# Performance work log

Hardware: AMD Instinct MI355X
Metric: run time of the kernel (lower is better)

## Reference

```python
import jax, jax.numpy as jnp
import numpy as np

B, S, D = 8, 4096, 192
MEM_READ, MEM_WRITE, MEM_READY = 156, 157, 158


def setup_inputs() -> dict:
    key = jax.random.key(0)
    ks = jax.random.split(key, 9)
    inp = {"x": jax.random.normal(ks[0], (B, S, D), dtype=jnp.float32)}
    names = ["Wq_r", "Wk_r", "Wv_r", "Wo_r", "Wq_w", "Wk_w", "Wv_w", "Wo_w"]
    for i, n in enumerate(names):
        inp[n] = jax.random.normal(ks[i + 1], (D, D), dtype=jnp.float32) * 0.02
    return inp


def _attention(x, Wq, Wk, Wv, Wo):
    # single-head, non-causal PureAttention: q/k/v = x @ W.T, softmax(qk^T/sqrt(D)) v, then W_o
    q = jnp.einsum('bsd,ed->bse', x, Wq)
    k = jnp.einsum('bsd,ed->bse', x, Wk)
    v = jnp.einsum('bsd,ed->bse', x, Wv)
    scale = jnp.asarray(1.0 / np.sqrt(D), x.dtype)
    scores = jnp.einsum('bqe,bke->bqk', q, k) * scale  # [B,S,S]
    attn = jax.nn.softmax(scores, axis=-1)
    o = jnp.einsum('bqk,bke->bqe', attn, v)
    return jnp.einsum('bse,oe->bso', o, Wo)


def reference(x, Wq_r, Wk_r, Wv_r, Wo_r, Wq_w, Wk_w, Wv_w, Wo_w):
    read_flag = x[:, 0, MEM_READ]    # [B]
    write_flag = x[:, 0, MEM_WRITE]  # [B]
    read_res = _attention(x, Wq_r, Wk_r, Wv_r, Wo_r)
    write_res = _attention(x, Wq_w, Wk_w, Wv_w, Wo_w)
    rg = read_flag[:, None, None]
    wg = write_flag[:, None, None]
    out = x + rg * (read_res - x) + wg * (write_res - x)
    out = out.at[:, :, MEM_READ].set(0.0)
    out = out.at[:, :, MEM_WRITE].set(0.0)
    ready = (read_flag + write_flag)[:, None]  # broadcast over seq
    out = out.at[:, :, MEM_READY].set(jnp.broadcast_to(ready, out.shape[:2]))
    return out
```

## Files before the change

kernel.cpp:

```cpp
#include <hip/hip_runtime.h>
#include <stdint.h>

#define B_ 8
#define S_ 4096
#define D_ 192
#define M_ (B_*S_)

typedef short v8s __attribute__((ext_vector_type(8)));
typedef float v4f __attribute__((ext_vector_type(4)));
typedef unsigned short v4us __attribute__((ext_vector_type(4)));
typedef unsigned long long ull;

static __device__ __forceinline__ unsigned short f2bf(float f){
  union{float f; unsigned u;} v; v.f=f;
  unsigned u = v.u;
  unsigned r = (u + 0x7fffu + ((u>>16)&1u))>>16;
  return (unsigned short)r;
}
static __device__ __forceinline__ float fexp2(float x){
  return __builtin_amdgcn_exp2f(x);
}
static __device__ __forceinline__ unsigned cvtpk(float lo, float hi){
  unsigned r;
  asm("v_cvt_pk_bf16_f32 %0, %1, %2" : "=v"(r) : "v"(lo), "v"(hi));
  return r;
}

static __device__ __forceinline__ unsigned sw_fp8(float x){
  union{float f; unsigned u;} v; v.f = x;
  unsigned s = (v.u >> 24) & 0x80u;
  float a = fabsf(x);
  if (a < 0.001953125f) return s;
  if (a >= 240.f) return s | 0x7Eu;
  if (a < 0.015625f) {
    int m = (int)(a*512.f + 0.5f); if(m>7) m=7;
    return s | (unsigned)m;
  }
  int e = (int)((v.u >> 23) & 0xff) - 127;
  unsigned mant = (v.u >> 20) & 0x7u;
  unsigned rest = v.u & 0xFFFFFu;
  if (rest > 0x80000u || (rest == 0x80000u && (mant&1u))) mant++;
  unsigned ee = (unsigned)(e + 7);
  if (mant == 8u){ mant = 0u; ee++; }
  return s | (ee<<3) | mant;
}
template<bool HI>
static __device__ __forceinline__ unsigned pk8(float a, float b, unsigned old){
#if __has_builtin(__builtin_amdgcn_cvt_pk_fp8_f32)
  return __builtin_amdgcn_cvt_pk_fp8_f32(a, b, old, HI);
#else
  unsigned p = sw_fp8(a) | (sw_fp8(b)<<8);
  return HI ? ((old & 0x0000FFFFu) | (p<<16)) : ((old & 0xFFFF0000u) | p);
#endif
}

typedef const __attribute__((address_space(1))) unsigned int gu32;
typedef __attribute__((address_space(3))) unsigned int lu32;
#define GLL16(gp, lp) __builtin_amdgcn_global_load_lds((gu32*)(gp), (lu32*)(lp), 16, 0, 0)

__global__ void cvt_w_kernel(const float* w0,const float* w1,const float* w2,const float* w3,
                             const float* w4,const float* w5,const float* w6,const float* w7,
                             unsigned short* dst){
  int w = blockIdx.y;
  const float* src;
  switch(w){
    case 0: src=w0; break; case 1: src=w1; break; case 2: src=w2; break; case 3: src=w3; break;
    case 4: src=w4; break; case 5: src=w5; break; case 6: src=w6; break; default: src=w7; break;
  }
  int i = blockIdx.x*256 + threadIdx.x;
  float v = src[i];
  if(w==0 || w==4 || w==1 || w==5) v *= 0.32267249f;
  dst[(size_t)w*36864 + i] = f2bf(v);
}

__global__ __launch_bounds__(256) void proj_kernel(
    const float* __restrict__ x, const unsigned short* __restrict__ Wb,
    unsigned char* __restrict__ QK8, unsigned short* __restrict__ V16)
{
  __shared__ __align__(16) unsigned short Vstage[192*72];
  const size_t MDB = (size_t)M_*D_;
  const size_t MD  = (size_t)M_*D_;
  int tid = threadIdx.x;
  int wid = tid>>6, lane = tid&63;
  int lr = lane&15, lg = lane>>4, kb = lg*8;
  int m0 = blockIdx.x*64 + wid*16;
  int row = m0 + lr;

  v8s a[6];
  #pragma unroll
  for(int c=0;c<6;c++){
    const float* xp = &x[(size_t)row*D_ + c*32 + kb];
    float4 f0 = *(const float4*)xp;
    float4 f1 = *(const float4*)(xp+4);
    v8s t;
    t[0]=(short)f2bf(f0.x); t[1]=(short)f2bf(f0.y); t[2]=(short)f2bf(f0.z); t[3]=(short)f2bf(f0.w);
    t[4]=(short)f2bf(f1.x); t[5]=(short)f2bf(f1.y); t[6]=(short)f2bf(f1.z); t[7]=(short)f2bf(f1.w);
    a[c]=t;
  }
  int bidx = m0 / S_;
  int sb   = (blockIdx.x*64) % S_;
  int sloc = wid*16 + lg*4;

  for(int path=0; path<2; path++){
    unsigned char* dstQ8 = QK8 + (size_t)path*2*MDB;
    for(int which=0; which<2; which++){
      const unsigned short* W = Wb + (size_t)(path*4 + which)*36864;
      unsigned char* dst = which==0 ? dstQ8 : dstQ8 + MDB;
      #pragma unroll
      for(int nt=0; nt<12; nt++){
        v4f acc = {0.f,0.f,0.f,0.f};
        int n = nt*16 + lr;
        #pragma unroll
        for(int c=0;c<6;c++){
          v8s bfr = *(const v8s*)&W[(size_t)n*D_ + c*32 + kb];
          acc = __builtin_amdgcn_mfma_f32_16x16x32_bf16(a[c], bfr, acc, 0,0,0);
        }
        int col = nt*16 + lr;
        int r0 = m0 + lg*4;
        #pragma unroll
        for(int r=0;r<4;r++){
          unsigned p = pk8<false>(acc[r], 0.f, 0u);
          dst[(size_t)(r0+r)*D_ + col] = (unsigned char)(p & 0xFF);
        }
      }
    }
    {
      const unsigned short* W = Wb + (size_t)(path*4 + 2)*36864;
      #pragma unroll
      for(int nt=0; nt<12; nt++){
        v4f acc = {0.f,0.f,0.f,0.f};
        int n = nt*16 + lr;
        #pragma unroll
        for(int c=0;c<6;c++){
          v8s bfr = *(const v8s*)&W[(size_t)n*D_ + c*32 + kb];
          acc = __builtin_amdgcn_mfma_f32_16x16x32_bf16(a[c], bfr, acc, 0,0,0);
        }
        int col = nt*16 + lr;
        v4us pk;
        pk[0]=f2bf(acc[0]); pk[1]=f2bf(acc[1]); pk[2]=f2bf(acc[2]); pk[3]=f2bf(acc[3]);
        *(v4us*)&Vstage[col*72 + sloc] = pk;
      }
      __syncthreads();
      unsigned short* dstV = V16 + (size_t)path*MD;
      size_t vg = (size_t)bidx*D_*S_ + sb;
      #pragma unroll
      for(int j=0;j<6;j++){
        int i = tid + j*256;
        int d = i>>3, s8 = (i&7)*8;
        *(v8s*)&dstV[vg + (size_t)d*S_ + s8] = *(const v8s*)&Vstage[d*72 + s8];
      }
      __syncthreads();
    }
  }
}

#define KSTR8 200

__global__ __launch_bounds__(256,3) void attn_kernel(
    const unsigned char* __restrict__ QK8,
    const unsigned short* __restrict__ V16,
    unsigned short* __restrict__ Ob)
{
  __shared__ __align__(16) unsigned char  KL[2][32*KSTR8];
  __shared__ __align__(16) unsigned short VL[2][192*32];

  int flat = blockIdx.x + 32*blockIdx.y + 256*blockIdx.z;
  int w = (flat&7)*64 + (flat>>3);
  int qi = w & 31;
  int b  = (w>>5) & 7;
  int z  = w>>8;

  const size_t MDB = (size_t)M_*D_;
  const unsigned char* Q8 = QK8 + (size_t)z*2*MDB;
  const unsigned char* K8 = Q8 + MDB;
  const unsigned short* Vt = V16 + (size_t)z*M_*D_;
  unsigned short* O = Ob + (size_t)z*M_*D_;

  int q0 = qi*128;
  int tid = threadIdx.x, wid=tid>>6, lane=tid&63;
  int lr = lane&15, lg = lane>>4;
  size_t bK = (size_t)b*S_*D_;
  size_t bV = (size_t)b*D_*S_;
  int qrow0 = q0 + wid*32;

  int ksR = tid>>3, ksC = (tid&7)*24;
  int kLds = ksR*KSTR8 + ksC;
  int voff[3], vLds[3];
  #pragma unroll
  for(int j=0;j<3;j++){
    int i = tid + j*256;
    int vrow = i>>2, vin = (i&3)*16;
    voff[j] = vrow*4096 + ((vin ^ (((vrow>>1)&3)<<4))>>1);
    vLds[j] = i*16;
  }
  int vro = ((lg*16) ^ (((lr>>1)&3)<<4)) >> 1;

  long qf8[2][6];
  #pragma unroll
  for(int h=0;h<2;h++){
    const unsigned char* qp = Q8 + bK + (size_t)(qrow0 + h*16 + lr)*D_;
    #pragma unroll
    for(int c=0;c<6;c++) qf8[h][c] = *(const long*)(qp + c*32 + lg*8);
  }
  float lsum[2] = {0.f, 0.f};
  v4f oacc[2][12];
  #pragma unroll
  for(int h=0;h<2;h++)
    #pragma unroll
    for(int e=0;e<12;e++) oacc[h][e] = (v4f){0.f,0.f,0.f,0.f};

  ull kreg0, kreg1, kreg2;
  auto kissue = [&](int t){
    const unsigned char* kg = K8 + bK + (size_t)t*6144 + ksR*192 + ksC;
    kreg0 = *(const ull*)(kg);
    kreg1 = *(const ull*)(kg+8);
    kreg2 = *(const ull*)(kg+16);
  };
  auto kwrite = [&](int buf){
    unsigned char* d = &KL[buf][kLds];
    *(ull*)(d)    = kreg0;
    *(ull*)(d+8)  = kreg1;
    *(ull*)(d+16) = kreg2;
  };
  auto vissue = [&](int t, int buf){
    const unsigned short* vg = Vt + bV + (size_t)t*32;
    #pragma unroll
    for(int j=0;j<3;j++) GLL16(vg + voff[j], ((unsigned char*)&VL[buf][0]) + vLds[j]);
  };
  auto do_qk = [&](int kcur, v4f sacc[2][2]){
    __builtin_amdgcn_s_setprio(1);
    #pragma unroll
    for(int ct=0; ct<2; ct++){
      v4f s0 = {0.f,0.f,0.f,0.f}, s1 = {0.f,0.f,0.f,0.f};
      const unsigned char* rb = &KL[kcur][(ct*16+lr)*KSTR8];
      #pragma unroll
      for(int c=0;c<6;c++){
        long kf8 = *(const long*)(rb + c*32 + lg*8);
        s0 = __builtin_amdgcn_mfma_f32_16x16x32_fp8_fp8(kf8, qf8[0][c], s0, 0,0,0);
        s1 = __builtin_amdgcn_mfma_f32_16x16x32_fp8_fp8(kf8, qf8[1][c], s1, 0,0,0);
      }
      sacc[0][ct]=s0; sacc[1][ct]=s1;
    }
    __builtin_amdgcn_s_setprio(0);
  };
  auto do_softmax = [&](v4f sacc[2][2], v8s pa[2]){
    #pragma unroll
    for(int h=0;h<2;h++){
      float p00=fexp2(sacc[h][0][0]), p01=fexp2(sacc[h][0][1]);
      float p02=fexp2(sacc[h][0][2]), p03=fexp2(sacc[h][0][3]);
      float p10=fexp2(sacc[h][1][0]), p11=fexp2(sacc[h][1][1]);
      float p12=fexp2(sacc[h][1][2]), p13=fexp2(sacc[h][1][3]);
      lsum[h] += ((p00+p01)+(p02+p03)) + ((p10+p11)+(p12+p13));
      unsigned X0=cvtpk(p00,p01), X1=cvtpk(p02,p03);
      unsigned Y0=cvtpk(p10,p11), Y1=cvtpk(p12,p13);
      asm("v_permlane32_swap_b32 %0, %1" : "+v"(Y0), "+v"(X0));
      asm("v_permlane32_swap_b32 %0, %1" : "+v"(Y1), "+v"(X1));
      asm("v_permlane16_swap_b32 %0, %1" : "+v"(Y0), "+v"(X0));
      asm("v_permlane16_swap_b32 %0, %1" : "+v"(Y1), "+v"(X1));
      union{ v8s s; unsigned w[4]; } u;
      u.w[0] = X0;  u.w[1] = X1;  u.w[2] = Y0;  u.w[3] = Y1;
      pa[h] = u.s;
    }
  };
  auto do_pv = [&](int vcur, v8s pa[2]){
    __builtin_amdgcn_s_setprio(1);
    #pragma unroll
    for(int e=0;e<12;e++){
      v8s vbf = *(const v8s*)&VL[vcur][(e*16+lr)*32 + vro];
      oacc[0][e] = __builtin_amdgcn_mfma_f32_16x16x32_bf16(pa[0], vbf, oacc[0][e], 0,0,0);
      oacc[1][e] = __builtin_amdgcn_mfma_f32_16x16x32_bf16(pa[1], vbf, oacc[1][e], 0,0,0);
    }
    __builtin_amdgcn_s_setprio(0);
  };

  kissue(0);
  vissue(0, 0);
  kwrite(0);
  asm volatile("s_waitcnt vmcnt(0)" ::: "memory");
  __syncthreads();

  for(int t=0; t<128; t++){
    int cur = t&1;
    if(t<127){ kissue(t+1); vissue(t+1, cur^1); }
    __builtin_amdgcn_sched_barrier(0);

    v4f sacc[2][2];
    do_qk(cur, sacc);
    v8s pa[2];
    do_softmax(sacc, pa);
    do_pv(cur, pa);

    if(t<127) kwrite(cur^1);
    asm volatile("s_waitcnt vmcnt(0)" ::: "memory");
    __syncthreads();
  }

  float invr[2][4];
  #pragma unroll
  for(int h=0;h<2;h++){
    float ps = lsum[h];
    ps += __shfl_xor(ps, 16);
    ps += __shfl_xor(ps, 32);
    float iv = 1.0f/ps;
    #pragma unroll
    for(int r=0;r<4;r++) invr[h][r] = __shfl(iv, lg*4+r, 16);
  }
  #pragma unroll
  for(int h=0;h<2;h++){
    size_t orow0 = ((size_t)b*S_ + qrow0 + h*16 + lg*4)*D_;
    #pragma unroll
    for(int e=0;e<12;e++){
      #pragma unroll
      for(int r=0;r<4;r++){
        O[orow0 + (size_t)r*D_ + e*16 + lr] = f2bf(oacc[h][e][r]*invr[h][r]);
      }
    }
  }
}

__global__ __launch_bounds__(256) void final_kernel(
  const float* __restrict__ x,
  const unsigned short* __restrict__ Or,
  const unsigned short* __restrict__ Ow,
  const unsigned short* __restrict__ WoR,
  const unsigned short* __restrict__ WoW,
  float* __restrict__ out)
{
  int tid=threadIdx.x, wid=tid>>6, lane=tid&63;
  int lr=lane&15, lg=lane>>4, kb=lg*8;
  int m0 = blockIdx.x*64 + wid*16;
  int arow = m0 + lr;
  v8s ar[6], aw[6];
  #pragma unroll
  for(int c=0;c<6;c++){
    ar[c] = *(const v8s*)&Or[(size_t)arow*D_ + c*32 + kb];
    aw[c] = *(const v8s*)&Ow[(size_t)arow*D_ + c*32 + kb];
  }
  int bidx = m0 / S_;
  float rf = x[(size_t)bidx*S_*D_ + 156];
  float wf = x[(size_t)bidx*S_*D_ + 157];
  #pragma unroll
  for(int nt=0; nt<12; nt++){
    v4f accR={0.f,0.f,0.f,0.f}, accW={0.f,0.f,0.f,0.f};
    int n = nt*16 + lr;
    #pragma unroll
    for(int c=0;c<6;c++){
      v8s br = *(const v8s*)&WoR[(size_t)n*D_ + c*32 + kb];
      accR = __builtin_amdgcn_mfma_f32_16x16x32_bf16(ar[c], br, accR,0,0,0);
      v8s bw = *(const v8s*)&WoW[(size_t)n*D_ + c*32 + kb];
      accW = __builtin_amdgcn_mfma_f32_16x16x32_bf16(aw[c], bw, accW,0,0,0);
    }
    #pragma unroll
    for(int r=0;r<4;r++){
      int row = m0 + lg*4 + r;
      int col = nt*16 + lr;
      float xv = x[(size_t)row*D_ + col];
      float val = xv + rf*(accR[r]-xv) + wf*(accW[r]-xv);
      if(col==156||col==157) val = 0.f;
      else if(col==158) val = rf+wf;
      out[(size_t)row*D_ + col] = val;
    }
  }
}

extern "C" void kernel_launch(void* const* d_in, const int* in_sizes, int n_in,
                              void* d_out, int out_size, void* d_ws, size_t ws_size,
                              hipStream_t stream) {
  const float* x = (const float*)d_in[0];
  char* wsb = (char*)d_ws;
  const size_t WSZ = 36864;
  const size_t MDB = (size_t)M_*D_;
  unsigned short* Wb  = (unsigned short*)wsb;
  unsigned char*  QK8 = (unsigned char*)(wsb + 8*WSZ*2);
  unsigned short* V16 = (unsigned short*)(wsb + 8*WSZ*2 + 4*MDB);
  unsigned short* Ob  = V16 + 2*MDB;

  cvt_w_kernel<<<dim3(144,8),256,0,stream>>>(
      (const float*)d_in[1],(const float*)d_in[2],(const float*)d_in[3],(const float*)d_in[4],
      (const float*)d_in[5],(const float*)d_in[6],(const float*)d_in[7],(const float*)d_in[8], Wb);

  proj_kernel<<<512,256,0,stream>>>(x, Wb, QK8, V16);
  attn_kernel<<<dim3(32,8,2),256,0,stream>>>(QK8, V16, Ob);
  final_kernel<<<512,256,0,stream>>>(x, Ob, Ob + MDB,
                                     Wb+3*WSZ, Wb+7*WSZ, (float*)d_out);
}
```

Baseline: 354.4 us.

## Split attention over two key halves and combine partials in final kernel

```diff
diff --git a/kernel.cpp b/kernel.cpp
--- a/kernel.cpp
+++ b/kernel.cpp
@@ -16,6 +16,9 @@
   unsigned u = v.u;
   unsigned r = (u + 0x7fffu + ((u>>16)&1u))>>16;
   return (unsigned short)r;
+}
+static __device__ __forceinline__ float bf2f(short s){
+  union{unsigned u; float f;} v; v.u = ((unsigned)(unsigned short)s)<<16; return v.f;
 }
 static __device__ __forceinline__ float fexp2(float x){
   return __builtin_amdgcn_exp2f(x);
@@ -156,25 +159,28 @@
 
 #define KSTR8 200
 
-__global__ __launch_bounds__(256,3) void attn_kernel(
+__global__ __launch_bounds__(256,4) void attn_kernel(
     const unsigned char* __restrict__ QK8,
     const unsigned short* __restrict__ V16,
-    unsigned short* __restrict__ Ob)
+    unsigned short* __restrict__ Ob,
+    float* __restrict__ Ls)
 {
   __shared__ __align__(16) unsigned char  KL[2][32*KSTR8];
   __shared__ __align__(16) unsigned short VL[2][192*32];
 
-  int flat = blockIdx.x + 32*blockIdx.y + 256*blockIdx.z;
-  int w = (flat&7)*64 + (flat>>3);
-  int qi = w & 31;
-  int b  = (w>>5) & 7;
-  int z  = w>>8;
+  int flat = blockIdx.x + 64*blockIdx.y + 512*blockIdx.z;
+  int w = (flat&7)*128 + (flat>>3);
+  int qi   =  w        & 31;
+  int b    = (w>>5)    & 7;
+  int z    = (w>>8)    & 1;
+  int half = (w>>9)    & 1;
 
   const size_t MDB = (size_t)M_*D_;
   const unsigned char* Q8 = QK8 + (size_t)z*2*MDB;
   const unsigned char* K8 = Q8 + MDB;
   const unsigned short* Vt = V16 + (size_t)z*M_*D_;
-  unsigned short* O = Ob + (size_t)z*M_*D_;
+  unsigned short* O = Ob + (size_t)(z*2+half)*MDB;
+  float* Lp = Ls + (size_t)(z*2+half)*M_;
 
   int q0 = qi*128;
   int tid = threadIdx.x, wid=tid>>6, lane=tid&63;
@@ -273,15 +279,17 @@
     __builtin_amdgcn_s_setprio(0);
   };
 
-  kissue(0);
-  vissue(0, 0);
+  int t0 = half*64;
+  kissue(t0);
+  vissue(t0, 0);
   kwrite(0);
   asm volatile("s_waitcnt vmcnt(0)" ::: "memory");
   __syncthreads();
 
-  for(int t=0; t<128; t++){
-    int cur = t&1;
-    if(t<127){ kissue(t+1); vissue(t+1, cur^1); }
+  for(int tt=0; tt<64; tt++){
+    int t = t0 + tt;
+    int cur = tt&1;
+    if(tt<63){ kissue(t+1); vissue(t+1, cur^1); }
     __builtin_amdgcn_sched_barrier(0);
 
     v4f sacc[2][2];
@@ -290,20 +298,19 @@
     do_softmax(sacc, pa);
     do_pv(cur, pa);
 
-    if(t<127) kwrite(cur^1);
+    if(tt<63) kwrite(cur^1);
     asm volatile("s_waitcnt vmcnt(0)" ::: "memory");
     __syncthreads();
   }
 
-  float invr[2][4];
   #pragma unroll
   for(int h=0;h<2;h++){
     float ps = lsum[h];
     ps += __shfl_xor(ps, 16);
     ps += __shfl_xor(ps, 32);
-    float iv = 1.0f/ps;
-    #pragma unroll
-    for(int r=0;r<4;r++) invr[h][r] = __shfl(iv, lg*4+r, 16);
+    if(lane < 16){
+      Lp[(size_t)b*S_ + qrow0 + h*16 + lr] = ps;
+    }
   }
   #pragma unroll
   for(int h=0;h<2;h++){
@@ -312,7 +319,7 @@
     for(int e=0;e<12;e++){
       #pragma unroll
       for(int r=0;r<4;r++){
-        O[orow0 + (size_t)r*D_ + e*16 + lr] = f2bf(oacc[h][e][r]*invr[h][r]);
+        O[orow0 + (size_t)r*D_ + e*16 + lr] = f2bf(oacc[h][e][r]);
       }
     }
   }
@@ -320,22 +327,40 @@
 
 __global__ __launch_bounds__(256) void final_kernel(
   const float* __restrict__ x,
-  const unsigned short* __restrict__ Or,
-  const unsigned short* __restrict__ Ow,
+  const unsigned short* __restrict__ Ob,
+  const float* __restrict__ Ls,
   const unsigned short* __restrict__ WoR,
   const unsigned short* __restrict__ WoW,
   float* __restrict__ out)
 {
+  const size_t MD = (size_t)M_*D_;
   int tid=threadIdx.x, wid=tid>>6, lane=tid&63;
   int lr=lane&15, lg=lane>>4, kb=lg*8;
   int m0 = blockIdx.x*64 + wid*16;
   int arow = m0 + lr;
+
   v8s ar[6], aw[6];
   #pragma unroll
-  for(int c=0;c<6;c++){
-    ar[c] = *(const v8s*)&Or[(size_t)arow*D_ + c*32 + kb];
-    aw[c] = *(const v8s*)&Ow[(size_t)arow*D_ + c*32 + kb];
-  }
+  for(int path=0; path<2; path++){
+    const unsigned short* O0 = Ob + (size_t)path*2*MD;
+    const unsigned short* O1 = O0 + MD;
+    const float* L0 = Ls + (size_t)path*2*M_;
+    const float* L1 = L0 + M_;
+    float inv = 1.0f/(L0[arow] + L1[arow]);
+    #pragma unroll
+    for(int c=0;c<6;c++){
+      v8s x0 = *(const v8s*)&O0[(size_t)arow*D_ + c*32 + kb];
+      v8s x1 = *(const v8s*)&O1[(size_t)arow*D_ + c*32 + kb];
+      v8s t;
+      #pragma unroll
+      for(int j=0;j<8;j++){
+        float f = (bf2f(x0[j]) + bf2f(x1[j])) * inv;
+        t[j] = (short)f2bf(f);
+      }
+      if(path==0) ar[c]=t; else aw[c]=t;
+    }
+  }
+
   int bidx = m0 / S_;
   float rf = x[(size_t)bidx*S_*D_ + 156];
   float wf = x[(size_t)bidx*S_*D_ + 157];
@@ -374,13 +399,14 @@
   unsigned char*  QK8 = (unsigned char*)(wsb + 8*WSZ*2);
   unsigned short* V16 = (unsigned short*)(wsb + 8*WSZ*2 + 4*MDB);
   unsigned short* Ob  = V16 + 2*MDB;
+  float*          Ls  = (float*)(Ob + 4*MDB);
 
   cvt_w_kernel<<<dim3(144,8),256,0,stream>>>(
       (const float*)d_in[1],(const float*)d_in[2],(const float*)d_in[3],(const float*)d_in[4],
       (const float*)d_in[5],(const float*)d_in[6],(const float*)d_in[7],(const float*)d_in[8], Wb);
 
   proj_kernel<<<512,256,0,stream>>>(x, Wb, QK8, V16);
-  attn_kernel<<<dim3(32,8,2),256,0,stream>>>(QK8, V16, Ob);
-  final_kernel<<<512,256,0,stream>>>(x, Ob, Ob + MDB,
+  attn_kernel<<<dim3(64,8,2),256,0,stream>>>(QK8, V16, Ob, Ls);
+  final_kernel<<<512,256,0,stream>>>(x, Ob, Ls,
                                      Wb+3*WSZ, Wb+7*WSZ, (float*)d_out);
 }
```

Result: slower. 1.067 ms (+201.2%).

## Use 512-thread attention blocks with split K/V loaders and software-pipelined PV

Applied to the files above, without the earlier changes.

```diff
diff --git a/kernel.cpp b/kernel.cpp
--- a/kernel.cpp
+++ b/kernel.cpp
@@ -156,13 +156,13 @@
 
 #define KSTR8 200
 
-__global__ __launch_bounds__(256,3) void attn_kernel(
+__global__ __launch_bounds__(512,4) void attn_kernel(
     const unsigned char* __restrict__ QK8,
     const unsigned short* __restrict__ V16,
     unsigned short* __restrict__ Ob)
 {
   __shared__ __align__(16) unsigned char  KL[2][32*KSTR8];
-  __shared__ __align__(16) unsigned short VL[2][192*32];
+  __shared__ __align__(16) unsigned short VL[3][192*32];
 
   int flat = blockIdx.x + 32*blockIdx.y + 256*blockIdx.z;
   int w = (flat&7)*64 + (flat>>3);
@@ -173,102 +173,102 @@
   const size_t MDB = (size_t)M_*D_;
   const unsigned char* Q8 = QK8 + (size_t)z*2*MDB;
   const unsigned char* K8 = Q8 + MDB;
-  const unsigned short* Vt = V16 + (size_t)z*M_*D_;
-  unsigned short* O = Ob + (size_t)z*M_*D_;
+  const unsigned short* Vt = V16 + (size_t)z*MDB;
+  unsigned short* O = Ob + (size_t)z*MDB;
 
   int q0 = qi*128;
   int tid = threadIdx.x, wid=tid>>6, lane=tid&63;
   int lr = lane&15, lg = lane>>4;
   size_t bK = (size_t)b*S_*D_;
   size_t bV = (size_t)b*D_*S_;
-  int qrow0 = q0 + wid*32;
-
-  int ksR = tid>>3, ksC = (tid&7)*24;
+  int qrow0 = q0 + wid*16;
+
+  bool isK = wid < 4;
+  int kt256 = tid & 255;
+  int ksR = kt256>>3, ksC = (kt256&7)*24;
   int kLds = ksR*KSTR8 + ksC;
   int voff[3], vLds[3];
   #pragma unroll
   for(int j=0;j<3;j++){
-    int i = tid + j*256;
+    int i = (tid & 255) + j*256;
     int vrow = i>>2, vin = (i&3)*16;
     voff[j] = vrow*4096 + ((vin ^ (((vrow>>1)&3)<<4))>>1);
     vLds[j] = i*16;
   }
   int vro = ((lg*16) ^ (((lr>>1)&3)<<4)) >> 1;
 
-  long qf8[2][6];
-  #pragma unroll
-  for(int h=0;h<2;h++){
-    const unsigned char* qp = Q8 + bK + (size_t)(qrow0 + h*16 + lr)*D_;
-    #pragma unroll
-    for(int c=0;c<6;c++) qf8[h][c] = *(const long*)(qp + c*32 + lg*8);
-  }
-  float lsum[2] = {0.f, 0.f};
-  v4f oacc[2][12];
-  #pragma unroll
-  for(int h=0;h<2;h++)
-    #pragma unroll
-    for(int e=0;e<12;e++) oacc[h][e] = (v4f){0.f,0.f,0.f,0.f};
-
-  ull kreg0, kreg1, kreg2;
+  long qf8[6];
+  {
+    const unsigned char* qp = Q8 + bK + (size_t)(qrow0 + lr)*D_;
+    #pragma unroll
+    for(int c=0;c<6;c++) qf8[c] = *(const long*)(qp + c*32 + lg*8);
+  }
+  float lsum = 0.f;
+  v4f oacc[12];
+  #pragma unroll
+  for(int e=0;e<12;e++) oacc[e] = (v4f){0.f,0.f,0.f,0.f};
+
+  ull k0, k1, k2;
   auto kissue = [&](int t){
-    const unsigned char* kg = K8 + bK + (size_t)t*6144 + ksR*192 + ksC;
-    kreg0 = *(const ull*)(kg);
-    kreg1 = *(const ull*)(kg+8);
-    kreg2 = *(const ull*)(kg+16);
+    if(isK){
+      const unsigned char* kg = K8 + bK + (size_t)t*6144 + ksR*192 + ksC;
+      k0 = *(const ull*)(kg);
+      k1 = *(const ull*)(kg+8);
+      k2 = *(const ull*)(kg+16);
+    }
   };
   auto kwrite = [&](int buf){
-    unsigned char* d = &KL[buf][kLds];
-    *(ull*)(d)    = kreg0;
-    *(ull*)(d+8)  = kreg1;
-    *(ull*)(d+16) = kreg2;
+    if(isK){
+      unsigned char* d = &KL[buf][kLds];
+      *(ull*)(d)    = k0;
+      *(ull*)(d+8)  = k1;
+      *(ull*)(d+16) = k2;
+    }
   };
   auto vissue = [&](int t, int buf){
-    const unsigned short* vg = Vt + bV + (size_t)t*32;
-    #pragma unroll
-    for(int j=0;j<3;j++) GLL16(vg + voff[j], ((unsigned char*)&VL[buf][0]) + vLds[j]);
-  };
-  auto do_qk = [&](int kcur, v4f sacc[2][2]){
+    if(!isK){
+      const unsigned short* vg = Vt + bV + (size_t)t*32;
+      #pragma unroll
+      for(int j=0;j<3;j++) GLL16(vg + voff[j], ((unsigned char*)&VL[buf][0]) + vLds[j]);
+    }
+  };
+  auto do_qk = [&](int kcur, v4f sacc[2]){
     __builtin_amdgcn_s_setprio(1);
     #pragma unroll
     for(int ct=0; ct<2; ct++){
-      v4f s0 = {0.f,0.f,0.f,0.f}, s1 = {0.f,0.f,0.f,0.f};
+      v4f s = {0.f,0.f,0.f,0.f};
       const unsigned char* rb = &KL[kcur][(ct*16+lr)*KSTR8];
       #pragma unroll
       for(int c=0;c<6;c++){
         long kf8 = *(const long*)(rb + c*32 + lg*8);
-        s0 = __builtin_amdgcn_mfma_f32_16x16x32_fp8_fp8(kf8, qf8[0][c], s0, 0,0,0);
-        s1 = __builtin_amdgcn_mfma_f32_16x16x32_fp8_fp8(kf8, qf8[1][c], s1, 0,0,0);
+        s = __builtin_amdgcn_mfma_f32_16x16x32_fp8_fp8(kf8, qf8[c], s, 0,0,0);
       }
-      sacc[0][ct]=s0; sacc[1][ct]=s1;
+      sacc[ct]=s;
     }
     __builtin_amdgcn_s_setprio(0);
   };
-  auto do_softmax = [&](v4f sacc[2][2], v8s pa[2]){
-    #pragma unroll
-    for(int h=0;h<2;h++){
-      float p00=fexp2(sacc[h][0][0]), p01=fexp2(sacc[h][0][1]);
-      float p02=fexp2(sacc[h][0][2]), p03=fexp2(sacc[h][0][3]);
-      float p10=fexp2(sacc[h][1][0]), p11=fexp2(sacc[h][1][1]);
-      float p12=fexp2(sacc[h][1][2]), p13=fexp2(sacc[h][1][3]);
-      lsum[h] += ((p00+p01)+(p02+p03)) + ((p10+p11)+(p12+p13));
-      unsigned X0=cvtpk(p00,p01), X1=cvtpk(p02,p03);
-      unsigned Y0=cvtpk(p10,p11), Y1=cvtpk(p12,p13);
-      asm("v_permlane32_swap_b32 %0, %1" : "+v"(Y0), "+v"(X0));
-      asm("v_permlane32_swap_b32 %0, %1" : "+v"(Y1), "+v"(X1));
-      asm("v_permlane16_swap_b32 %0, %1" : "+v"(Y0), "+v"(X0));
-      asm("v_permlane16_swap_b32 %0, %1" : "+v"(Y1), "+v"(X1));
-      union{ v8s s; unsigned w[4]; } u;
-      u.w[0] = X0;  u.w[1] = X1;  u.w[2] = Y0;  u.w[3] = Y1;
-      pa[h] = u.s;
-    }
-  };
-  auto do_pv = [&](int vcur, v8s pa[2]){
+  auto do_softmax = [&](v4f sacc[2], v8s& pa){
+    float p00=fexp2(sacc[0][0]), p01=fexp2(sacc[0][1]);
+    float p02=fexp2(sacc[0][2]), p03=fexp2(sacc[0][3]);
+    float p10=fexp2(sacc[1][0]), p11=fexp2(sacc[1][1]);
+    float p12=fexp2(sacc[1][2]), p13=fexp2(sacc[1][3]);
+    lsum += ((p00+p01)+(p02+p03)) + ((p10+p11)+(p12+p13));
+    unsigned X0=cvtpk(p00,p01), X1=cvtpk(p02,p03);
+    unsigned Y0=cvtpk(p10,p11), Y1=cvtpk(p12,p13);
+    asm("v_permlane32_swap_b32 %0, %1" : "+v"(Y0), "+v"(X0));
+    asm("v_permlane32_swap_b32 %0, %1" : "+v"(Y1), "+v"(X1));
+    asm("v_permlane16_swap_b32 %0, %1" : "+v"(Y0), "+v"(X0));
+    asm("v_permlane16_swap_b32 %0, %1" : "+v"(Y1), "+v"(X1));
+    union{ v8s s; unsigned w[4]; } u;
+    u.w[0] = X0;  u.w[1] = X1;  u.w[2] = Y0;  u.w[3] = Y1;
+    pa = u.s;
+  };
+  auto do_pv = [&](int vcur, v8s pa){
     __builtin_amdgcn_s_setprio(1);
     #pragma unroll
     for(int e=0;e<12;e++){
       v8s vbf = *(const v8s*)&VL[vcur][(e*16+lr)*32 + vro];
-      oacc[0][e] = __builtin_amdgcn_mfma_f32_16x16x32_bf16(pa[0], vbf, oacc[0][e], 0,0,0);
-      oacc[1][e] = __builtin_amdgcn_mfma_f32_16x16x32_bf16(pa[1], vbf, oacc[1][e], 0,0,0);
+      oacc[e] = __builtin_amdgcn_mfma_f32_16x16x32_bf16(pa, vbf, oacc[e], 0,0,0);
     }
     __builtin_amdgcn_s_setprio(0);
   };
@@ -279,41 +279,45 @@
   asm volatile("s_waitcnt vmcnt(0)" ::: "memory");
   __syncthreads();
 
-  for(int t=0; t<128; t++){
-    int cur = t&1;
-    if(t<127){ kissue(t+1); vissue(t+1, cur^1); }
+  v8s pa_prev;
+  {
+    v4f sacc[2];
+    do_qk(0, sacc);
+    kissue(1);
+    vissue(1, 1);
     __builtin_amdgcn_sched_barrier(0);
-
-    v4f sacc[2][2];
-    do_qk(cur, sacc);
-    v8s pa[2];
-    do_softmax(sacc, pa);
-    do_pv(cur, pa);
-
-    if(t<127) kwrite(cur^1);
+    do_softmax(sacc, pa_prev);
+    kwrite(1);
     asm volatile("s_waitcnt vmcnt(0)" ::: "memory");
     __syncthreads();
   }
 
-  float invr[2][4];
-  #pragma unroll
-  for(int h=0;h<2;h++){
-    float ps = lsum[h];
-    ps += __shfl_xor(ps, 16);
-    ps += __shfl_xor(ps, 32);
-    float iv = 1.0f/ps;
-    #pragma unroll
-    for(int r=0;r<4;r++) invr[h][r] = __shfl(iv, lg*4+r, 16);
-  }
-  #pragma unroll
-  for(int h=0;h<2;h++){
-    size_t orow0 = ((size_t)b*S_ + qrow0 + h*16 + lg*4)*D_;
-    #pragma unroll
-    for(int e=0;e<12;e++){
-      #pragma unroll
-      for(int r=0;r<4;r++){
-        O[orow0 + (size_t)r*D_ + e*16 + lr] = f2bf(oacc[h][e][r]*invr[h][r]);
-      }
+  for(int t=1; t<128; t++){
+    v4f sacc[2];
+    do_qk(t&1, sacc);
+    if(t<127){ kissue(t+1); vissue(t+1, (t+1)%3); }
+    __builtin_amdgcn_sched_barrier(0);
+    do_pv((t-1)%3, pa_prev);
+    do_softmax(sacc, pa_prev);
+    if(t<127) kwrite((t+1)&1);
+    asm volatile("s_waitcnt vmcnt(0)" ::: "memory");
+    __syncthreads();
+  }
+  do_pv(127%3, pa_prev);
+
+  float ps = lsum;
+  ps += __shfl_xor(ps, 16);
+  ps += __shfl_xor(ps, 32);
+  float iv = 1.0f/ps;
+  float invr[4];
+  #pragma unroll
+  for(int r=0;r<4;r++) invr[r] = __shfl(iv, lg*4+r, 16);
+  size_t orow0 = ((size_t)b*S_ + qrow0 + lg*4)*D_;
+  #pragma unroll
+  for(int e=0;e<12;e++){
+    #pragma unroll
+    for(int r=0;r<4;r++){
+      O[orow0 + (size_t)r*D_ + e*16 + lr] = f2bf(oacc[e][r]*invr[r]);
     }
   }
 }
@@ -380,7 +384,7 @@
       (const float*)d_in[5],(const float*)d_in[6],(const float*)d_in[7],(const float*)d_in[8], Wb);
 
   proj_kernel<<<512,256,0,stream>>>(x, Wb, QK8, V16);
-  attn_kernel<<<dim3(32,8,2),256,0,stream>>>(QK8, V16, Ob);
+  attn_kernel<<<dim3(32,8,2),512,0,stream>>>(QK8, V16, Ob);
   final_kernel<<<512,256,0,stream>>>(x, Ob, Ob + MDB,
                                      Wb+3*WSZ, Wb+7*WSZ, (float*)d_out);
 }
```

Result: faster. 335.1 us (-5.4%).
